# Kernel tuning notes

Hardware: AMD Instinct MI355X
Metric: run time of the kernel (lower is better)

The kernel has to match this reference:

```python
import jax, jax.numpy as jnp
import numpy as np

B, S, D = 128, 512, 768          # batch, seq_len, token_dim
NH, HD = 8, 96                    # num_heads, head_dim = sentence_dim/num_heads
HID = 4 * HD                      # hidden_dim = 384


def setup_inputs() -> dict:
    key = jax.random.key(0)
    ks = jax.random.split(key, 9)
    token_embeddings = jax.random.normal(ks[0], (B, S, D), dtype=jnp.float32)
    # variable-length attention mask (1 for real tokens, 0 for padding)
    lengths = jax.random.randint(ks[1], (B,), S // 2, S + 1)
    attention_mask = (jnp.arange(S)[None, :] < lengths[:, None]).astype(jnp.float32)
    s = 0.02
    P  = jax.random.normal(ks[2], (NH, HD, D),   dtype=jnp.float32) * s
    bP = jnp.zeros((NH, HD), dtype=jnp.float32)
    W1 = jax.random.normal(ks[3], (NH, HID, HD), dtype=jnp.float32) * s
    b1 = jnp.zeros((NH, HID), dtype=jnp.float32)
    W2 = jax.random.normal(ks[4], (NH, HD, HID), dtype=jnp.float32) * s
    b2 = jnp.zeros((NH, HD), dtype=jnp.float32)
    return {"token_embeddings": token_embeddings, "attention_mask": attention_mask,
            "P": P, "bP": bP, "W1": W1, "b1": b1, "W2": W2, "b2": b2}


def reference(token_embeddings, attention_mask, P, bP, W1, b1, W2, b2):
    # per-head projection: H_i = P_i(H)           -> (nh, B, S, HD)
    Hi = jnp.einsum('bsd,ihd->ibsh', token_embeddings, P) + bP[:, None, None, :]
    # scores: W2(relu(W1(H_i)))                   -> (nh, B, S, HD)
    A = jnp.einsum('ibsf,ihf->ibsh',
                   jax.nn.relu(jnp.einsum('ibsh,ifh->ibsf', Hi, W1) + b1[:, None, None, :]),
                   W2) + b2[:, None, None, :]
    # masked softmax over sequence dim (log(mask) adds -inf on padding)
    log_mask = jnp.log(attention_mask)[None, :, :, None]  # (1, B, S, 1)
    A = jax.nn.softmax(A + log_mask, axis=2)
    # weighted sum over tokens                    -> (nh, B, HD)
    v = jnp.sum(Hi * A, axis=2)
    # concat heads: (B, nh*HD) = (B, 768)
    pooled = jnp.transpose(v, (1, 0, 2)).reshape(token_embeddings.shape[0], NH * HD)
    return pooled
```

## Files before the change

kernel.cpp:

```cpp
#include <hip/hip_runtime.h>
#include <stdint.h>


typedef short bf16x8 __attribute__((ext_vector_type(8)));
typedef float f32x4 __attribute__((ext_vector_type(4)));

struct alignas(8) us4 { unsigned short x, y, z, w; };

__device__ __forceinline__ unsigned short f32_to_bf16(float f) {
  union { float f; uint32_t u; } v; v.f = f;
  uint32_t u = v.u;
  uint32_t r = (u + 0x7fffu + ((u >> 16) & 1u)) >> 16;
  return (unsigned short)r;
}

__device__ __forceinline__ float bf16_to_f32(unsigned short h) {
  union { uint32_t u; float f; } v; v.u = ((uint32_t)h) << 16;
  return v.f;
}

__device__ __forceinline__ uint32_t pack_bf16_trunc(float lo, float hi) {
  union { float f; uint32_t u; } a, b; a.f = lo; b.f = hi;
  return __builtin_amdgcn_perm(b.u, a.u, 0x07060302u);
}

__device__ __forceinline__ void g2l16(const unsigned short* g, unsigned short* l) {
  __builtin_amdgcn_global_load_lds((__attribute__((address_space(1))) void*)g,
                                   (__attribute__((address_space(3))) void*)l,
                                   16, 0, 0);
}


#define N_X   50331648
#define N_P   589824
#define N_W1  294912
#define N_W2  294912
#define N_HI  50331648


__global__ __launch_bounds__(256) void cast_f32_bf16(
    const float* __restrict__ src, unsigned short* __restrict__ dst, int n4) {
  int idx = blockIdx.x * 256 + threadIdx.x;
  if (idx >= n4) return;
  float4 v = ((const float4*)src)[idx];
  us4 o;
  o.x = f32_to_bf16(v.x);
  o.y = f32_to_bf16(v.y);
  o.z = f32_to_bf16(v.z);
  o.w = f32_to_bf16(v.w);
  ((us4*)dst)[idx] = o;
}


__global__ __launch_bounds__(256) void gemm_hi(
    const unsigned short* __restrict__ Xbf,
    const unsigned short* __restrict__ Pbf,
    const float* __restrict__ bP,
    unsigned short* __restrict__ Hi) {
  __shared__ __align__(16) unsigned short As[128 * 32];
  __shared__ __align__(16) unsigned short Bs[128 * 32];

  const int tid = threadIdx.x;
  const int w = tid >> 6;
  const int lane = tid & 63;
  const int r = lane & 15;
  const int q = lane >> 4;
  const int bn = blockIdx.x;
  const int bm = blockIdx.y;
  const int wr = w >> 1, wc = w & 1;

  f32x4 acc[4][4];
#pragma unroll
  for (int a = 0; a < 4; ++a)
#pragma unroll
    for (int c = 0; c < 4; ++c) acc[a][c] = (f32x4){0.f, 0.f, 0.f, 0.f};

  const int ldr = lane >> 2;
  const int ldc = (lane & 3) * 8;
  const unsigned short* Abase = Xbf + (size_t)(bm * 128) * 768 + ldc;
  const unsigned short* Bbase = Pbf + (size_t)(bn * 128) * 768 + ldc;

  for (int k0 = 0; k0 < 768; k0 += 32) {
    __syncthreads();
    g2l16(Abase + (size_t)(w * 16 + ldr) * 768 + k0, &As[w * 512]);
    g2l16(Abase + (size_t)(64 + w * 16 + ldr) * 768 + k0, &As[(4 + w) * 512]);
    g2l16(Bbase + (size_t)(w * 16 + ldr) * 768 + k0, &Bs[w * 512]);
    g2l16(Bbase + (size_t)(64 + w * 16 + ldr) * 768 + k0, &Bs[(4 + w) * 512]);
    __syncthreads();

    bf16x8 af[4], bfr[4];
#pragma unroll
    for (int t = 0; t < 4; ++t)
      af[t] = *(const bf16x8*)&As[(wr * 64 + t * 16 + r) * 32 + q * 8];
#pragma unroll
    for (int t = 0; t < 4; ++t)
      bfr[t] = *(const bf16x8*)&Bs[(wc * 64 + t * 16 + r) * 32 + q * 8];
#pragma unroll
    for (int mt = 0; mt < 4; ++mt)
#pragma unroll
      for (int nt = 0; nt < 4; ++nt)
        acc[mt][nt] = __builtin_amdgcn_mfma_f32_16x16x32_bf16(
            af[mt], bfr[nt], acc[mt][nt], 0, 0, 0);
  }

  const int bb = bm >> 2;
  const int sb = (bm & 3) * 128 + wr * 64;
#pragma unroll
  for (int nt = 0; nt < 4; ++nt) {
    const int n0 = bn * 128 + wc * 64 + nt * 16;
    const int hd = n0 / 96;
    const int h = n0 - hd * 96 + r;
    const float bias = bP[n0 + r];
    unsigned short* obase = Hi + (size_t)(hd * 128 + bb) * 512 * 96 + h;
#pragma unroll
    for (int mt = 0; mt < 4; ++mt) {
#pragma unroll
      for (int rg = 0; rg < 4; ++rg) {
        const int s = sb + mt * 16 + q * 4 + rg;
        obase[(size_t)s * 96] = f32_to_bf16(acc[mt][nt][rg] + bias);
      }
    }
  }
}


__global__ __launch_bounds__(256, 2) void mlp_pool(
    const unsigned short* __restrict__ Hi,
    const unsigned short* __restrict__ W1bf,
    const unsigned short* __restrict__ W2bf,
    const float* __restrict__ b1,
    const float* __restrict__ b2,
    const float* __restrict__ mask,
    float* __restrict__ out) {
  __shared__ __align__(16) unsigned short Ys[128 * 96];
  __shared__ __align__(16) unsigned short Ws[96 * 96];
  __shared__ __align__(16) unsigned short Fs[128 * 104];
  __shared__ __align__(16) float b1s[384];
  __shared__ __align__(16) float b2s[96];
  __shared__ float bias_s[512];
  __shared__ float redA[4][96];
  __shared__ float redB[4][96];

  const int x = blockIdx.x;
  const int b = x & 127;
  const int hd = x >> 7;

  const int tid = threadIdx.x;
  const int w = tid >> 6;
  const int lane = tid & 63;
  const int r = lane & 15;
  const int q = lane >> 4;

  if (tid < 96) b2s[tid] = b2[hd * 96 + tid];
  for (int i = tid; i < 384; i += 256) b1s[i] = b1[hd * 384 + i];
  for (int s = tid; s < 512; s += 256)
    bias_s[s] = mask[b * 512 + s] > 0.5f ? 0.f : -1e30f;

  float m_run[6], l_run[6], v_run[6];
#pragma unroll
  for (int nt = 0; nt < 6; ++nt) { m_run[nt] = -3e30f; l_run[nt] = 0.f; v_run[nt] = 0.f; }

  for (int c = 0; c < 4; ++c) {
    __syncthreads();

    const unsigned short* ysrc =
        Hi + ((size_t)(hd * 128 + b) * 512 + c * 128) * 96;
#pragma unroll
    for (int it = 0; it < 6; ++it)
      g2l16(ysrc + (size_t)((it * 4 + w) * 64 + lane) * 8, &Ys[(it * 4 + w) * 512]);

    f32x4 acc3[2][6];
#pragma unroll
    for (int sp = 0; sp < 2; ++sp)
#pragma unroll
      for (int nt = 0; nt < 6; ++nt) acc3[sp][nt] = (f32x4){0.f, 0.f, 0.f, 0.f};

    for (int ph = 0; ph < 4; ++ph) {
      __syncthreads();
      const unsigned short* w1src = W1bf + ((size_t)hd * 384 + ph * 96) * 96;
#pragma unroll
      for (int it = 0; it < 4; ++it)
        g2l16(w1src + (size_t)((it * 4 + w) * 64 + lane) * 8, &Ws[(it * 4 + w) * 512]);
      if (w < 2)
        g2l16(w1src + (size_t)((16 + w) * 64 + lane) * 8, &Ws[(16 + w) * 512]);
      __syncthreads();

      f32x4 acc2[6][2];
#pragma unroll
      for (int ft = 0; ft < 6; ++ft)
#pragma unroll
        for (int sp = 0; sp < 2; ++sp) acc2[ft][sp] = (f32x4){0.f, 0.f, 0.f, 0.f};
#pragma unroll
      for (int kb = 0; kb < 3; ++kb) {
        bf16x8 bfrg[2];
#pragma unroll
        for (int sp = 0; sp < 2; ++sp)
          bfrg[sp] = *(const bf16x8*)&Ys[((w * 2 + sp) * 16 + r) * 96 + kb * 32 + q * 8];
#pragma unroll
        for (int ft = 0; ft < 6; ++ft) {
          bf16x8 afrg = *(const bf16x8*)&Ws[(ft * 16 + r) * 96 + kb * 32 + q * 8];
#pragma unroll
          for (int sp = 0; sp < 2; ++sp)
            acc2[ft][sp] = __builtin_amdgcn_mfma_f32_16x16x32_bf16(
                afrg, bfrg[sp], acc2[ft][sp], 0, 0, 0);
        }
      }
#pragma unroll
      for (int ft = 0; ft < 6; ++ft) {
        float4 bv = *(const float4*)&b1s[ph * 96 + ft * 16 + q * 4];
#pragma unroll
        for (int sp = 0; sp < 2; ++sp) {
          const int s = (w * 2 + sp) * 16 + r;
          float v0 = fmaxf(acc2[ft][sp][0] + bv.x, 0.f);
          float v1 = fmaxf(acc2[ft][sp][1] + bv.y, 0.f);
          float v2 = fmaxf(acc2[ft][sp][2] + bv.z, 0.f);
          float v3 = fmaxf(acc2[ft][sp][3] + bv.w, 0.f);
          uint2 pk;
          pk.x = pack_bf16_trunc(v0, v1);
          pk.y = pack_bf16_trunc(v2, v3);
          *(uint2*)((uint32_t*)&Fs[0] + s * 52 + ft * 8 + q * 2) = pk;
        }
      }
      __syncthreads();

      const unsigned short* w2src = W2bf + (size_t)hd * 96 * 384 + ph * 96;
#pragma unroll
      for (int it = 0; it < 4; ++it) {
        const int ch = (it * 4 + w) * 64 + lane;
        const int kb = ch / 384;
        const int rem = ch - kb * 384;
        g2l16(w2src + (size_t)(rem >> 2) * 384 + kb * 32 + (rem & 3) * 8,
              &Ws[(it * 4 + w) * 512]);
      }
      if (w < 2) {
        const int ch = (16 + w) * 64 + lane;
        const int kb = ch / 384;
        const int rem = ch - kb * 384;
        g2l16(w2src + (size_t)(rem >> 2) * 384 + kb * 32 + (rem & 3) * 8,
              &Ws[(16 + w) * 512]);
      }
      __syncthreads();

#pragma unroll
      for (int kb = 0; kb < 3; ++kb) {
        bf16x8 afrg[2];
#pragma unroll
        for (int sp = 0; sp < 2; ++sp)
          afrg[sp] = *(const bf16x8*)&Fs[((w * 2 + sp) * 16 + r) * 104 + kb * 32 + q * 8];
#pragma unroll
        for (int nt = 0; nt < 6; ++nt) {
          bf16x8 bfrg = *(const bf16x8*)&Ws[(kb * 96 + nt * 16 + r) * 32 + q * 8];
#pragma unroll
          for (int sp = 0; sp < 2; ++sp)
            acc3[sp][nt] = __builtin_amdgcn_mfma_f32_16x16x32_bf16(
                afrg[sp], bfrg, acc3[sp][nt], 0, 0, 0);
        }
      }
    }

#pragma unroll
    for (int nt = 0; nt < 6; ++nt) {
      const int h = nt * 16 + r;
      const float b2v = b2s[h];
      float lm = -3e30f;
#pragma unroll
      for (int sp = 0; sp < 2; ++sp) {
#pragma unroll
        for (int rg = 0; rg < 4; ++rg) {
          const int sl = (w * 2 + sp) * 16 + q * 4 + rg;
          float lg = acc3[sp][nt][rg] + b2v + bias_s[c * 128 + sl];
          lm = fmaxf(lm, lg);
        }
      }
      lm = fmaxf(lm, __shfl_xor(lm, 16));
      lm = fmaxf(lm, __shfl_xor(lm, 32));
      if (q == 0) redA[w][h] = lm;
    }
    __syncthreads();
#pragma unroll
    for (int nt = 0; nt < 6; ++nt) {
      const int h = nt * 16 + r;
      const float cm = fmaxf(fmaxf(redA[0][h], redA[1][h]),
                             fmaxf(redA[2][h], redA[3][h]));
      const float mnew = fmaxf(m_run[nt], cm);
      const float sc = __expf(m_run[nt] - mnew);
      m_run[nt] = mnew;
      float lacc = l_run[nt] * sc;
      float vacc = v_run[nt] * sc;
      const float b2v = b2s[h];
#pragma unroll
      for (int sp = 0; sp < 2; ++sp) {
#pragma unroll
        for (int rg = 0; rg < 4; ++rg) {
          const int sl = (w * 2 + sp) * 16 + q * 4 + rg;
          float lg = acc3[sp][nt][rg] + b2v + bias_s[c * 128 + sl];
          float e = __expf(lg - mnew);
          lacc += e;
          vacc += e * bf16_to_f32(Ys[sl * 96 + h]);
        }
      }
      l_run[nt] = lacc;
      v_run[nt] = vacc;
    }
  }

  __syncthreads();
#pragma unroll
  for (int nt = 0; nt < 6; ++nt) {
    float ls = l_run[nt], vs = v_run[nt];
    ls += __shfl_xor(ls, 16);
    vs += __shfl_xor(vs, 16);
    ls += __shfl_xor(ls, 32);
    vs += __shfl_xor(vs, 32);
    if (q == 0) {
      redA[w][nt * 16 + r] = ls;
      redB[w][nt * 16 + r] = vs;
    }
  }
  __syncthreads();
  if (tid < 96) {
    float ls = redA[0][tid] + redA[1][tid] + redA[2][tid] + redA[3][tid];
    float vs = redB[0][tid] + redB[1][tid] + redB[2][tid] + redB[3][tid];
    out[(size_t)b * 768 + hd * 96 + tid] = vs / ls;
  }
}


extern "C" void kernel_launch(void* const* d_in, const int* in_sizes, int n_in,
                              void* d_out, int out_size, void* d_ws, size_t ws_size,
                              hipStream_t stream) {
  const float* X    = (const float*)d_in[0];
  const float* mask = (const float*)d_in[1];
  const float* P    = (const float*)d_in[2];
  const float* bP   = (const float*)d_in[3];
  const float* W1   = (const float*)d_in[4];
  const float* b1   = (const float*)d_in[5];
  const float* W2   = (const float*)d_in[6];
  const float* b2   = (const float*)d_in[7];
  float* out = (float*)d_out;
  (void)in_sizes; (void)n_in; (void)out_size; (void)ws_size;

  unsigned short* Xbf  = (unsigned short*)d_ws;
  unsigned short* Pbf  = Xbf + N_X;
  unsigned short* W1bf = Pbf + N_P;
  unsigned short* W2bf = W1bf + N_W1;
  unsigned short* Hi   = W2bf + N_W2;

  cast_f32_bf16<<<N_X / 4 / 256, 256, 0, stream>>>(X, Xbf, N_X / 4);
  cast_f32_bf16<<<N_P / 4 / 256, 256, 0, stream>>>(P, Pbf, N_P / 4);
  cast_f32_bf16<<<N_W1 / 4 / 256, 256, 0, stream>>>(W1, W1bf, N_W1 / 4);
  cast_f32_bf16<<<N_W2 / 4 / 256, 256, 0, stream>>>(W2, W2bf, N_W2 / 4);

  gemm_hi<<<dim3(6, 512), 256, 0, stream>>>(Xbf, Pbf, bP, Hi);
  mlp_pool<<<8 * 128, 256, 0, stream>>>(Hi, W1bf, W2bf, b1, b2, mask, out);
}
```

Baseline: 534.4 us.

## Swizzle LDS tiles and overlap W2 load with W1 GEMM in MLP

Applies an XOR swizzle to the 16-byte chunks of the shared-memory tiles in both kernels, so MFMA fragment reads avoid LDS bank conflicts. In the MLP kernel, W2 gets its own buffer, which lets its load be issued before the W1 GEMM instead of after the ReLU store. The W1 tile and the F activations now share one buffer. The Y fragments are held in registers across phases, which raises register pressure under the 2-block occupancy bound and adds an extra barrier.

```diff
diff --git a/kernel.cpp b/kernel.cpp
--- a/kernel.cpp
+++ b/kernel.cpp
@@ -68,6 +68,7 @@
   const int bn = blockIdx.x;
   const int bm = blockIdx.y;
   const int wr = w >> 1, wc = w & 1;
+  const int psw = q ^ ((r >> 1) & 3);
 
   f32x4 acc[4][4];
 #pragma unroll
@@ -76,7 +77,7 @@
     for (int c = 0; c < 4; ++c) acc[a][c] = (f32x4){0.f, 0.f, 0.f, 0.f};
 
   const int ldr = lane >> 2;
-  const int ldc = (lane & 3) * 8;
+  const int ldc = ((lane & 3) ^ ((lane >> 3) & 3)) * 8;
   const unsigned short* Abase = Xbf + (size_t)(bm * 128) * 768 + ldc;
   const unsigned short* Bbase = Pbf + (size_t)(bn * 128) * 768 + ldc;
 
@@ -91,10 +92,10 @@
     bf16x8 af[4], bfr[4];
 #pragma unroll
     for (int t = 0; t < 4; ++t)
-      af[t] = *(const bf16x8*)&As[(wr * 64 + t * 16 + r) * 32 + q * 8];
+      af[t] = *(const bf16x8*)&As[(wr * 64 + t * 16 + r) * 32 + psw * 8];
 #pragma unroll
     for (int t = 0; t < 4; ++t)
-      bfr[t] = *(const bf16x8*)&Bs[(wc * 64 + t * 16 + r) * 32 + q * 8];
+      bfr[t] = *(const bf16x8*)&Bs[(wc * 64 + t * 16 + r) * 32 + psw * 8];
 #pragma unroll
     for (int mt = 0; mt < 4; ++mt)
 #pragma unroll
@@ -133,8 +134,8 @@
     const float* __restrict__ mask,
     float* __restrict__ out) {
   __shared__ __align__(16) unsigned short Ys[128 * 96];
-  __shared__ __align__(16) unsigned short Ws[96 * 96];
-  __shared__ __align__(16) unsigned short Fs[128 * 104];
+  __shared__ __align__(16) unsigned short U[128 * 104];
+  __shared__ __align__(16) unsigned short Ws2[3 * 96 * 32];
   __shared__ __align__(16) float b1s[384];
   __shared__ __align__(16) float b2s[96];
   __shared__ float bias_s[512];
@@ -150,6 +151,7 @@
   const int lane = tid & 63;
   const int r = lane & 15;
   const int q = lane >> 4;
+  const int psw = q ^ ((r >> 1) & 3);
 
   if (tid < 96) b2s[tid] = b2[hd * 96 + tid];
   for (int i = tid; i < 384; i += 256) b1s[i] = b1[hd * 384 + i];
@@ -166,8 +168,14 @@
     const unsigned short* ysrc =
         Hi + ((size_t)(hd * 128 + b) * 512 + c * 128) * 96;
 #pragma unroll
-    for (int it = 0; it < 6; ++it)
-      g2l16(ysrc + (size_t)((it * 4 + w) * 64 + lane) * 8, &Ys[(it * 4 + w) * 512]);
+    for (int it = 0; it < 6; ++it) {
+      const int ch = (it * 4 + w) * 64 + lane;
+      const int row = ch / 12;
+      const int g = ch - row * 12;
+      const int kb = g >> 2, p = g & 3;
+      g2l16(ysrc + (size_t)row * 96 + kb * 32 + (p ^ ((row >> 1) & 3)) * 8,
+            &Ys[(it * 4 + w) * 512]);
+    }
 
     f32x4 acc3[2][6];
 #pragma unroll
@@ -175,15 +183,58 @@
 #pragma unroll
       for (int nt = 0; nt < 6; ++nt) acc3[sp][nt] = (f32x4){0.f, 0.f, 0.f, 0.f};
 
+    bf16x8 yfrg[2][3];
+
     for (int ph = 0; ph < 4; ++ph) {
+      if (ph) __syncthreads();
+
+      const unsigned short* w1src = W1bf + ((size_t)hd * 384 + ph * 96) * 96;
+#pragma unroll
+      for (int it = 0; it < 4; ++it) {
+        const int ch = (it * 4 + w) * 64 + lane;
+        const int row = ch / 12;
+        const int g = ch - row * 12;
+        const int kb = g >> 2, p = g & 3;
+        g2l16(w1src + (size_t)row * 96 + kb * 32 + (p ^ ((row >> 1) & 3)) * 8,
+              &U[(it * 4 + w) * 512]);
+      }
+      if (w < 2) {
+        const int ch = 1024 + w * 64 + lane;
+        const int row = ch / 12;
+        const int g = ch - row * 12;
+        const int kb = g >> 2, p = g & 3;
+        g2l16(w1src + (size_t)row * 96 + kb * 32 + (p ^ ((row >> 1) & 3)) * 8,
+              &U[(16 + w) * 512]);
+      }
       __syncthreads();
-      const unsigned short* w1src = W1bf + ((size_t)hd * 384 + ph * 96) * 96;
-#pragma unroll
-      for (int it = 0; it < 4; ++it)
-        g2l16(w1src + (size_t)((it * 4 + w) * 64 + lane) * 8, &Ws[(it * 4 + w) * 512]);
-      if (w < 2)
-        g2l16(w1src + (size_t)((16 + w) * 64 + lane) * 8, &Ws[(16 + w) * 512]);
-      __syncthreads();
+
+      const unsigned short* w2src = W2bf + (size_t)hd * 96 * 384 + ph * 96;
+#pragma unroll
+      for (int it = 0; it < 4; ++it) {
+        const int ch = (it * 4 + w) * 64 + lane;
+        const int kb = ch / 384;
+        const int rem = ch - kb * 384;
+        const int hh = rem >> 2, p = rem & 3;
+        g2l16(w2src + (size_t)hh * 384 + kb * 32 + (p ^ ((hh >> 1) & 3)) * 8,
+              &Ws2[(it * 4 + w) * 512]);
+      }
+      if (w < 2) {
+        const int ch = 1024 + w * 64 + lane;
+        const int kb = ch / 384;
+        const int rem = ch - kb * 384;
+        const int hh = rem >> 2, p = rem & 3;
+        g2l16(w2src + (size_t)hh * 384 + kb * 32 + (p ^ ((hh >> 1) & 3)) * 8,
+              &Ws2[(16 + w) * 512]);
+      }
+
+      if (ph == 0) {
+#pragma unroll
+        for (int sp = 0; sp < 2; ++sp)
+#pragma unroll
+          for (int kb = 0; kb < 3; ++kb)
+            yfrg[sp][kb] =
+                *(const bf16x8*)&Ys[((w * 2 + sp) * 16 + r) * 96 + kb * 32 + psw * 8];
+      }
 
       f32x4 acc2[6][2];
 #pragma unroll
@@ -192,19 +243,17 @@
         for (int sp = 0; sp < 2; ++sp) acc2[ft][sp] = (f32x4){0.f, 0.f, 0.f, 0.f};
 #pragma unroll
       for (int kb = 0; kb < 3; ++kb) {
-        bf16x8 bfrg[2];
-#pragma unroll
-        for (int sp = 0; sp < 2; ++sp)
-          bfrg[sp] = *(const bf16x8*)&Ys[((w * 2 + sp) * 16 + r) * 96 + kb * 32 + q * 8];
 #pragma unroll
         for (int ft = 0; ft < 6; ++ft) {
-          bf16x8 afrg = *(const bf16x8*)&Ws[(ft * 16 + r) * 96 + kb * 32 + q * 8];
+          bf16x8 afrg = *(const bf16x8*)&U[(ft * 16 + r) * 96 + kb * 32 + psw * 8];
 #pragma unroll
           for (int sp = 0; sp < 2; ++sp)
             acc2[ft][sp] = __builtin_amdgcn_mfma_f32_16x16x32_bf16(
-                afrg, bfrg[sp], acc2[ft][sp], 0, 0, 0);
-        }
-      }
+                afrg, yfrg[sp][kb], acc2[ft][sp], 0, 0, 0);
+        }
+      }
+      __syncthreads();
+
 #pragma unroll
       for (int ft = 0; ft < 6; ++ft) {
         float4 bv = *(const float4*)&b1s[ph * 96 + ft * 16 + q * 4];
@@ -218,26 +267,8 @@
           uint2 pk;
           pk.x = pack_bf16_trunc(v0, v1);
           pk.y = pack_bf16_trunc(v2, v3);
-          *(uint2*)((uint32_t*)&Fs[0] + s * 52 + ft * 8 + q * 2) = pk;
-        }
-      }
-      __syncthreads();
-
-      const unsigned short* w2src = W2bf + (size_t)hd * 96 * 384 + ph * 96;
-#pragma unroll
-      for (int it = 0; it < 4; ++it) {
-        const int ch = (it * 4 + w) * 64 + lane;
-        const int kb = ch / 384;
-        const int rem = ch - kb * 384;
-        g2l16(w2src + (size_t)(rem >> 2) * 384 + kb * 32 + (rem & 3) * 8,
-              &Ws[(it * 4 + w) * 512]);
-      }
-      if (w < 2) {
-        const int ch = (16 + w) * 64 + lane;
-        const int kb = ch / 384;
-        const int rem = ch - kb * 384;
-        g2l16(w2src + (size_t)(rem >> 2) * 384 + kb * 32 + (rem & 3) * 8,
-              &Ws[(16 + w) * 512]);
+          *(uint2*)((uint32_t*)&U[0] + s * 52 + ft * 8 + q * 2) = pk;
+        }
       }
       __syncthreads();
 
@@ -246,10 +277,10 @@
         bf16x8 afrg[2];
 #pragma unroll
         for (int sp = 0; sp < 2; ++sp)
-          afrg[sp] = *(const bf16x8*)&Fs[((w * 2 + sp) * 16 + r) * 104 + kb * 32 + q * 8];
+          afrg[sp] = *(const bf16x8*)&U[((w * 2 + sp) * 16 + r) * 104 + kb * 32 + q * 8];
 #pragma unroll
         for (int nt = 0; nt < 6; ++nt) {
-          bf16x8 bfrg = *(const bf16x8*)&Ws[(kb * 96 + nt * 16 + r) * 32 + q * 8];
+          bf16x8 bfrg = *(const bf16x8*)&Ws2[(kb * 96 + nt * 16 + r) * 32 + psw * 8];
 #pragma unroll
           for (int sp = 0; sp < 2; ++sp)
             acc3[sp][nt] = __builtin_amdgcn_mfma_f32_16x16x32_bf16(
@@ -280,6 +311,9 @@
 #pragma unroll
     for (int nt = 0; nt < 6; ++nt) {
       const int h = nt * 16 + r;
+      const int gh = nt * 2 + (r >> 3);
+      const int kbh = gh >> 2, ph_ = gh & 3;
+      const int hlo = r & 7;
       const float cm = fmaxf(fmaxf(redA[0][h], redA[1][h]),
                              fmaxf(redA[2][h], redA[3][h]));
       const float mnew = fmaxf(m_run[nt], cm);
@@ -296,7 +330,8 @@
           float lg = acc3[sp][nt][rg] + b2v + bias_s[c * 128 + sl];
           float e = __expf(lg - mnew);
           lacc += e;
-          vacc += e * bf16_to_f32(Ys[sl * 96 + h]);
+          const int pos = ph_ ^ ((sl >> 1) & 3);
+          vacc += e * bf16_to_f32(Ys[sl * 96 + kbh * 32 + pos * 8 + hlo]);
         }
       }
       l_run[nt] = lacc;
```

Result: slower. 567.7 us (+6.2%).

## Swizzle LDS layouts and repack Hi/W1/W2 into k-blocked XOR-swizzled tiles

Applied to the files above, without the earlier changes.

Applies an XOR swizzle to the 16-byte column slots of the shared-memory tiles in gemm_hi and mlp_pool, aimed at removing LDS bank conflicts on the MFMA fragment reads. Hi is rewritten in a k-blocked layout of 32-column slabs, and W1/W2 are converted by new repack kernels into pre-swizzled per-quarter tiles, so each tile loads as contiguous global chunks. The value gather in the softmax step is reindexed to match. It adds address arithmetic and more coupled index logic, which raises the risk of indexing mistakes.

```diff
diff --git a/kernel.cpp b/kernel.cpp
--- a/kernel.cpp
+++ b/kernel.cpp
@@ -52,6 +52,49 @@
 }
 
 
+__global__ __launch_bounds__(256) void repack_w1(
+    const float* __restrict__ W1, unsigned short* __restrict__ W1bf) {
+  const int quarter = blockIdx.x;
+  const int hd = quarter >> 2, ph = quarter & 3;
+  for (int t = threadIdx.x; t < 1152; t += 256) {
+    const int kb = t / 384;
+    const int rem = t - kb * 384;
+    const int f = rem >> 2, slot = rem & 3;
+    const int pos = slot ^ ((f >> 1) & 3);
+    const float* src =
+        W1 + ((size_t)(hd * 384 + ph * 96 + f)) * 96 + kb * 32 + pos * 8;
+    float4 a = *(const float4*)src;
+    float4 b = *(const float4*)(src + 4);
+    us4 o1 = {f32_to_bf16(a.x), f32_to_bf16(a.y), f32_to_bf16(a.z), f32_to_bf16(a.w)};
+    us4 o2 = {f32_to_bf16(b.x), f32_to_bf16(b.y), f32_to_bf16(b.z), f32_to_bf16(b.w)};
+    us4* dst = (us4*)(W1bf + (size_t)quarter * 9216 + t * 8);
+    dst[0] = o1;
+    dst[1] = o2;
+  }
+}
+
+__global__ __launch_bounds__(256) void repack_w2(
+    const float* __restrict__ W2, unsigned short* __restrict__ W2bf) {
+  const int quarter = blockIdx.x;
+  const int hd = quarter >> 2, ph = quarter & 3;
+  for (int t = threadIdx.x; t < 1152; t += 256) {
+    const int kb = t / 384;
+    const int rem = t - kb * 384;
+    const int h = rem >> 2, slot = rem & 3;
+    const int pos = slot ^ ((h >> 1) & 3);
+    const float* src =
+        W2 + ((size_t)(hd * 96 + h)) * 384 + ph * 96 + kb * 32 + pos * 8;
+    float4 a = *(const float4*)src;
+    float4 b = *(const float4*)(src + 4);
+    us4 o1 = {f32_to_bf16(a.x), f32_to_bf16(a.y), f32_to_bf16(a.z), f32_to_bf16(a.w)};
+    us4 o2 = {f32_to_bf16(b.x), f32_to_bf16(b.y), f32_to_bf16(b.z), f32_to_bf16(b.w)};
+    us4* dst = (us4*)(W2bf + (size_t)quarter * 9216 + t * 8);
+    dst[0] = o1;
+    dst[1] = o2;
+  }
+}
+
+
 __global__ __launch_bounds__(256) void gemm_hi(
     const unsigned short* __restrict__ Xbf,
     const unsigned short* __restrict__ Pbf,
@@ -68,6 +111,7 @@
   const int bn = blockIdx.x;
   const int bm = blockIdx.y;
   const int wr = w >> 1, wc = w & 1;
+  const int psw = q ^ ((r >> 1) & 3);
 
   f32x4 acc[4][4];
 #pragma unroll
@@ -76,7 +120,7 @@
     for (int c = 0; c < 4; ++c) acc[a][c] = (f32x4){0.f, 0.f, 0.f, 0.f};
 
   const int ldr = lane >> 2;
-  const int ldc = (lane & 3) * 8;
+  const int ldc = ((lane & 3) ^ ((lane >> 3) & 3)) * 8;
   const unsigned short* Abase = Xbf + (size_t)(bm * 128) * 768 + ldc;
   const unsigned short* Bbase = Pbf + (size_t)(bn * 128) * 768 + ldc;
 
@@ -91,10 +135,10 @@
     bf16x8 af[4], bfr[4];
 #pragma unroll
     for (int t = 0; t < 4; ++t)
-      af[t] = *(const bf16x8*)&As[(wr * 64 + t * 16 + r) * 32 + q * 8];
+      af[t] = *(const bf16x8*)&As[(wr * 64 + t * 16 + r) * 32 + psw * 8];
 #pragma unroll
     for (int t = 0; t < 4; ++t)
-      bfr[t] = *(const bf16x8*)&Bs[(wc * 64 + t * 16 + r) * 32 + q * 8];
+      bfr[t] = *(const bf16x8*)&Bs[(wc * 64 + t * 16 + r) * 32 + psw * 8];
 #pragma unroll
     for (int mt = 0; mt < 4; ++mt)
 #pragma unroll
@@ -109,15 +153,18 @@
   for (int nt = 0; nt < 4; ++nt) {
     const int n0 = bn * 128 + wc * 64 + nt * 16;
     const int hd = n0 / 96;
-    const int h = n0 - hd * 96 + r;
+    const int hloc = n0 - hd * 96;
+    const int kb = hloc >> 5;
+    const int col = (hloc & 31) + r;
     const float bias = bP[n0 + r];
-    unsigned short* obase = Hi + (size_t)(hd * 128 + bb) * 512 * 96 + h;
+    unsigned short* obase =
+        Hi + (size_t)(hd * 128 + bb) * 49152 + kb * 16384 + col;
 #pragma unroll
     for (int mt = 0; mt < 4; ++mt) {
 #pragma unroll
       for (int rg = 0; rg < 4; ++rg) {
         const int s = sb + mt * 16 + q * 4 + rg;
-        obase[(size_t)s * 96] = f32_to_bf16(acc[mt][nt][rg] + bias);
+        obase[(size_t)s * 32] = f32_to_bf16(acc[mt][nt][rg] + bias);
       }
     }
   }
@@ -132,8 +179,8 @@
     const float* __restrict__ b2,
     const float* __restrict__ mask,
     float* __restrict__ out) {
-  __shared__ __align__(16) unsigned short Ys[128 * 96];
-  __shared__ __align__(16) unsigned short Ws[96 * 96];
+  __shared__ __align__(16) unsigned short Ys[3 * 128 * 32];
+  __shared__ __align__(16) unsigned short Ws[3 * 96 * 32];
   __shared__ __align__(16) unsigned short Fs[128 * 104];
   __shared__ __align__(16) float b1s[384];
   __shared__ __align__(16) float b2s[96];
@@ -150,6 +197,8 @@
   const int lane = tid & 63;
   const int r = lane & 15;
   const int q = lane >> 4;
+  const int psw = q ^ ((r >> 1) & 3);
+  const int ysx = (tid ^ ((tid >> 3) & 3)) * 8;
 
   if (tid < 96) b2s[tid] = b2[hd * 96 + tid];
   for (int i = tid; i < 384; i += 256) b1s[i] = b1[hd * 384 + i];
@@ -160,14 +209,20 @@
 #pragma unroll
   for (int nt = 0; nt < 6; ++nt) { m_run[nt] = -3e30f; l_run[nt] = 0.f; v_run[nt] = 0.f; }
 
+  const unsigned short* ysrc = Hi + (size_t)(hd * 128 + b) * 49152;
+
   for (int c = 0; c < 4; ++c) {
     __syncthreads();
 
-    const unsigned short* ysrc =
-        Hi + ((size_t)(hd * 128 + b) * 512 + c * 128) * 96;
-#pragma unroll
-    for (int it = 0; it < 6; ++it)
-      g2l16(ysrc + (size_t)((it * 4 + w) * 64 + lane) * 8, &Ys[(it * 4 + w) * 512]);
+    {
+      const unsigned short* yc = ysrc + c * 4096 + ysx;
+      g2l16(yc, &Ys[w * 512]);
+      g2l16(yc + 2048, &Ys[(4 + w) * 512]);
+      g2l16(yc + 16384, &Ys[(8 + w) * 512]);
+      g2l16(yc + 18432, &Ys[(12 + w) * 512]);
+      g2l16(yc + 32768, &Ys[(16 + w) * 512]);
+      g2l16(yc + 34816, &Ys[(20 + w) * 512]);
+    }
 
     f32x4 acc3[2][6];
 #pragma unroll
@@ -176,8 +231,9 @@
       for (int nt = 0; nt < 6; ++nt) acc3[sp][nt] = (f32x4){0.f, 0.f, 0.f, 0.f};
 
     for (int ph = 0; ph < 4; ++ph) {
-      __syncthreads();
-      const unsigned short* w1src = W1bf + ((size_t)hd * 384 + ph * 96) * 96;
+      if (ph) __syncthreads();
+
+      const unsigned short* w1src = W1bf + (size_t)(hd * 4 + ph) * 9216;
 #pragma unroll
       for (int it = 0; it < 4; ++it)
         g2l16(w1src + (size_t)((it * 4 + w) * 64 + lane) * 8, &Ws[(it * 4 + w) * 512]);
@@ -195,10 +251,10 @@
         bf16x8 bfrg[2];
 #pragma unroll
         for (int sp = 0; sp < 2; ++sp)
-          bfrg[sp] = *(const bf16x8*)&Ys[((w * 2 + sp) * 16 + r) * 96 + kb * 32 + q * 8];
+          bfrg[sp] = *(const bf16x8*)&Ys[kb * 4096 + ((w * 2 + sp) * 16 + r) * 32 + psw * 8];
 #pragma unroll
         for (int ft = 0; ft < 6; ++ft) {
-          bf16x8 afrg = *(const bf16x8*)&Ws[(ft * 16 + r) * 96 + kb * 32 + q * 8];
+          bf16x8 afrg = *(const bf16x8*)&Ws[kb * 3072 + (ft * 16 + r) * 32 + psw * 8];
 #pragma unroll
           for (int sp = 0; sp < 2; ++sp)
             acc2[ft][sp] = __builtin_amdgcn_mfma_f32_16x16x32_bf16(
@@ -223,22 +279,12 @@
       }
       __syncthreads();
 
-      const unsigned short* w2src = W2bf + (size_t)hd * 96 * 384 + ph * 96;
-#pragma unroll
-      for (int it = 0; it < 4; ++it) {
-        const int ch = (it * 4 + w) * 64 + lane;
-        const int kb = ch / 384;
-        const int rem = ch - kb * 384;
-        g2l16(w2src + (size_t)(rem >> 2) * 384 + kb * 32 + (rem & 3) * 8,
-              &Ws[(it * 4 + w) * 512]);
-      }
-      if (w < 2) {
-        const int ch = (16 + w) * 64 + lane;
-        const int kb = ch / 384;
-        const int rem = ch - kb * 384;
-        g2l16(w2src + (size_t)(rem >> 2) * 384 + kb * 32 + (rem & 3) * 8,
-              &Ws[(16 + w) * 512]);
-      }
+      const unsigned short* w2src = W2bf + (size_t)(hd * 4 + ph) * 9216;
+#pragma unroll
+      for (int it = 0; it < 4; ++it)
+        g2l16(w2src + (size_t)((it * 4 + w) * 64 + lane) * 8, &Ws[(it * 4 + w) * 512]);
+      if (w < 2)
+        g2l16(w2src + (size_t)((16 + w) * 64 + lane) * 8, &Ws[(16 + w) * 512]);
       __syncthreads();
 
 #pragma unroll
@@ -249,7 +295,7 @@
           afrg[sp] = *(const bf16x8*)&Fs[((w * 2 + sp) * 16 + r) * 104 + kb * 32 + q * 8];
 #pragma unroll
         for (int nt = 0; nt < 6; ++nt) {
-          bf16x8 bfrg = *(const bf16x8*)&Ws[(kb * 96 + nt * 16 + r) * 32 + q * 8];
+          bf16x8 bfrg = *(const bf16x8*)&Ws[kb * 3072 + (nt * 16 + r) * 32 + psw * 8];
 #pragma unroll
           for (int sp = 0; sp < 2; ++sp)
             acc3[sp][nt] = __builtin_amdgcn_mfma_f32_16x16x32_bf16(
@@ -260,8 +306,7 @@
 
 #pragma unroll
     for (int nt = 0; nt < 6; ++nt) {
-      const int h = nt * 16 + r;
-      const float b2v = b2s[h];
+      const float b2v = b2s[nt * 16 + r];
       float lm = -3e30f;
 #pragma unroll
       for (int sp = 0; sp < 2; ++sp) {
@@ -274,12 +319,15 @@
       }
       lm = fmaxf(lm, __shfl_xor(lm, 16));
       lm = fmaxf(lm, __shfl_xor(lm, 32));
-      if (q == 0) redA[w][h] = lm;
+      if (q == 0) redA[w][nt * 16 + r] = lm;
     }
     __syncthreads();
 #pragma unroll
     for (int nt = 0; nt < 6; ++nt) {
       const int h = nt * 16 + r;
+      const int kbh = nt >> 1;
+      const int gh = (nt * 2 + (r >> 3)) & 3;
+      const int hlo = r & 7;
       const float cm = fmaxf(fmaxf(redA[0][h], redA[1][h]),
                              fmaxf(redA[2][h], redA[3][h]));
       const float mnew = fmaxf(m_run[nt], cm);
@@ -296,7 +344,8 @@
           float lg = acc3[sp][nt][rg] + b2v + bias_s[c * 128 + sl];
           float e = __expf(lg - mnew);
           lacc += e;
-          vacc += e * bf16_to_f32(Ys[sl * 96 + h]);
+          const int pos = gh ^ ((sl >> 1) & 3);
+          vacc += e * bf16_to_f32(Ys[kbh * 4096 + sl * 32 + pos * 8 + hlo]);
         }
       }
       l_run[nt] = lacc;
@@ -348,8 +397,8 @@
 
   cast_f32_bf16<<<N_X / 4 / 256, 256, 0, stream>>>(X, Xbf, N_X / 4);
   cast_f32_bf16<<<N_P / 4 / 256, 256, 0, stream>>>(P, Pbf, N_P / 4);
-  cast_f32_bf16<<<N_W1 / 4 / 256, 256, 0, stream>>>(W1, W1bf, N_W1 / 4);
-  cast_f32_bf16<<<N_W2 / 4 / 256, 256, 0, stream>>>(W2, W2bf, N_W2 / 4);
+  repack_w1<<<32, 256, 0, stream>>>(W1, W1bf);
+  repack_w2<<<32, 256, 0, stream>>>(W2, W2bf);
 
   gemm_hi<<<dim3(6, 512), 256, 0, stream>>>(Xbf, Pbf, bP, Hi);
   mlp_pool<<<8 * 128, 256, 0, stream>>>(Hi, W1bf, W2bf, b1, b2, mask, out);
```

Result: no change. 525.4 us (-1.7%).
